# Performance work log

Measured on AMD Instinct MI355X. Metric: run time of the kernel, lower is better.

## Reference

```python
import jax, jax.numpy as jnp
import numpy as np

NUM_EMBEDDINGS = 512
EMBEDDING_DIM = 64
COMMITMENT_COST = 0.25
DECAY = 0.99
EPSILON = 1e-05


def setup_inputs() -> dict:
    key = jax.random.key(0)
    k1, k2, k3 = jax.random.split(key, 3)
    inputs = jax.random.normal(k1, (32, 64, 64, EMBEDDING_DIM), dtype=jnp.float32)
    emb_w = jax.random.normal(k2, (NUM_EMBEDDINGS, EMBEDDING_DIM), dtype=jnp.float32)
    ema_cluster_size = jnp.ones((NUM_EMBEDDINGS,), dtype=jnp.float32)
    ema_w = jax.random.normal(k3, (NUM_EMBEDDINGS, EMBEDDING_DIM), dtype=jnp.float32)
    return {"inputs": inputs, "emb_w": emb_w,
            "ema_cluster_size": ema_cluster_size, "ema_w": ema_w}


def reference(inputs, emb_w, ema_cluster_size, ema_w):
    """VQ-VAE EMA quantizer forward (training=True path).

    inputs:           [B, H, W, D]  NHWC latents
    emb_w:            [K, D]        codebook (pre-update)
    ema_cluster_size: [K]           EMA cluster-size buffer
    ema_w:            [K, D]        EMA weight buffer
    """
    B, H, W, D = inputs.shape
    K = emb_w.shape[0]
    flat = inputs.reshape(-1, D)                                  # [N, D]

    distances = (jnp.sum(flat * flat, axis=1, keepdims=True)
                 - 2.0 * flat @ emb_w.T
                 + jnp.sum(emb_w * emb_w, axis=1))
    encoding_indices = jnp.argmin(distances, axis=1)              # [N]
    encodings = jax.nn.one_hot(encoding_indices, K, dtype=flat.dtype)  # [N, K]

    # --- EMA codebook update (buffer math; no gradient flows here) ---
    counts = jax.lax.stop_gradient(jnp.sum(encodings, axis=0))    # [K]
    cs = ema_cluster_size * DECAY + (1.0 - DECAY) * counts
    n = jnp.sum(cs)
    cs = (cs + EPSILON) / (n + K * EPSILON) * n                   # Laplace smoothing
    dw = jax.ops.segment_sum(jax.lax.stop_gradient(flat),
                             encoding_indices, num_segments=K)    # [K, D]
    new_ema_w = ema_w * DECAY + (1.0 - DECAY) * dw
    new_emb = new_ema_w / cs[:, None]                             # updated codebook

    # Quantize with the updated codebook (gather)
    quantized = new_emb[encoding_indices].reshape(B, H, W, D)

    # Commitment loss (quantized is detached)
    e_latent_loss = jnp.mean((jax.lax.stop_gradient(quantized) - inputs) ** 2)
    loss = COMMITMENT_COST * e_latent_loss

    # Straight-through estimator
    quantized_st = inputs + jax.lax.stop_gradient(quantized - inputs)

    avg_probs = jnp.mean(encodings, axis=0)
    perplexity = jnp.exp(-jnp.sum(avg_probs * jnp.log(avg_probs + 1e-10)))

    # NHWC -> NCHW as in the original return
    return loss, jnp.transpose(quantized_st, (0, 3, 1, 2)), perplexity, encodings
```

## Files before the change

### kernel.cpp

```cpp
#include <hip/hip_runtime.h>

#define DIM 64
#define K_CODES 512
#define N_VEC 131072
#define CREP 16
#define DREP 64
#define Q_OFF 1
#define PERP_OFF 8388609
#define ENC_OFF 8388610

#define DW_BLOCKS 512
#define ENC_BLOCKS 1280

using bfrag = __attribute__((ext_vector_type(8))) short;
using ffrag = __attribute__((ext_vector_type(4))) float;

__device__ __forceinline__ void split3(float x, short& h0, short& h1, short& h2)
{
    unsigned u0 = __float_as_uint(x);
    h0 = (short)(u0 >> 16);
    float r = x - __uint_as_float(u0 & 0xFFFF0000u);
    unsigned u1 = __float_as_uint(r);
    h1 = (short)(u1 >> 16);
    float r2 = r - __uint_as_float(u1 & 0xFFFF0000u);
    h2 = (short)(__float_as_uint(r2) >> 16);
}

__global__ __launch_bounds__(256) void epack_ee_kernel(
    const float* __restrict__ emb_w,
    bfrag* __restrict__ epack,
    float* __restrict__ ee,
    float* __restrict__ crep,
    float* __restrict__ lossac)
{
    __shared__ float part[2][16][8];
    const int tl = threadIdx.x;
    const int t = blockIdx.x * 256 + tl;
    const int lane = t & 63;
    const int db = (t >> 6) & 1;
    const int ctl = tl >> 7;
    const int ct = t >> 7;
    const int r16 = lane & 15, quad = lane >> 4;
    const int c  = ct * 16 + r16;
    const int d0 = db * 32 + quad * 8;
    const float* src = emb_w + (size_t)c * DIM + d0;

    crep[t] = 0.f;
    crep[4096 + t] = 0.f;
    if (t == 0) lossac[0] = 0.f;

    bfrag f0, f1, f2;
    float ssum = 0.f;
#pragma unroll
    for (int j = 0; j < 8; ++j) {
        const float x = src[j];
        ssum = fmaf(x, x, ssum);
        short a, b, cc;
        split3(x, a, b, cc);
        f0[j] = a; f1[j] = b; f2[j] = cc;
    }
    const int base = (ct * 2 + db) * 3;
    epack[(base + 0) * 64 + lane] = f0;
    epack[(base + 1) * 64 + lane] = f1;
    epack[(base + 2) * 64 + lane] = f2;

    part[ctl][r16][db * 4 + quad] = ssum;
    __syncthreads();
    if (tl < 32) {
        const int cl = tl >> 4, r = tl & 15;
        float s = 0.f;
#pragma unroll
        for (int i = 0; i < 8; ++i) s += part[cl][r][i];
        ee[(blockIdx.x * 2 + cl) * 16 + r] = s;
    }
}

__global__ __launch_bounds__(256, 2) void argmin_mfma_kernel(
    const float* __restrict__ inputs,
    const bfrag* __restrict__ epack,
    const float* __restrict__ eeg,
    int* __restrict__ idx,
    float* __restrict__ counts_rep,
    float* __restrict__ dwrep)
{
    const int t = threadIdx.x;
    const int lane = t & 63;
    const int r16 = lane & 15;
    const int quad = lane >> 4;
    const size_t v0 = (size_t)blockIdx.x * 256 + (t >> 6) * 64;

    {
        float4* z4 = reinterpret_cast<float4*>(dwrep) + (size_t)blockIdx.x * 1024;
        const float4 z = make_float4(0.f, 0.f, 0.f, 0.f);
#pragma unroll
        for (int i = 0; i < 4; ++i) z4[i * 256 + t] = z;
    }

    bfrag xf[4][2][3];
#pragma unroll
    for (int rt = 0; rt < 4; ++rt)
#pragma unroll
        for (int db = 0; db < 2; ++db) {
            const float* src = inputs + (v0 + rt * 16 + r16) * DIM + db * 32 + quad * 8;
            const float4 va = *reinterpret_cast<const float4*>(src);
            const float4 vb = *reinterpret_cast<const float4*>(src + 4);
            float vals[8] = {va.x, va.y, va.z, va.w, vb.x, vb.y, vb.z, vb.w};
            bfrag f0, f1, f2;
#pragma unroll
            for (int j = 0; j < 8; ++j) {
                short a, b, c;
                split3(vals[j], a, b, c);
                f0[j] = a; f1[j] = b; f2[j] = c;
            }
            xf[rt][db][0] = f0; xf[rt][db][1] = f1; xf[rt][db][2] = f2;
        }

    float best[4][4];
    int bestk[4][4];
#pragma unroll
    for (int a = 0; a < 4; ++a)
#pragma unroll
        for (int b = 0; b < 4; ++b) { best[a][b] = 3.4e38f; bestk[a][b] = 0; }

    constexpr int PI[6] = {0, 0, 1, 0, 2, 1};
    constexpr int PJ[6] = {0, 1, 0, 2, 0, 1};

#pragma unroll 2
    for (int ct = 0; ct < 32; ++ct) {
        bfrag e[2][3];
#pragma unroll
        for (int db = 0; db < 2; ++db)
#pragma unroll
            for (int s = 0; s < 3; ++s)
                e[db][s] = epack[((ct * 2 + db) * 3 + s) * 64 + lane];
        const float eel = eeg[ct * 16 + r16];

        ffrag acc[4];
#pragma unroll
        for (int rt = 0; rt < 4; ++rt) acc[rt] = (ffrag){0.f, 0.f, 0.f, 0.f};

#pragma unroll
        for (int db = 0; db < 2; ++db)
#pragma unroll
            for (int p = 0; p < 6; ++p)
#pragma unroll
                for (int rt = 0; rt < 4; ++rt)
                    acc[rt] = __builtin_amdgcn_mfma_f32_16x16x32_bf16(
                        xf[rt][db][PI[p]], e[db][PJ[p]], acc[rt], 0, 0, 0);

        const int kc = ct * 16 + r16;
#pragma unroll
        for (int rt = 0; rt < 4; ++rt)
#pragma unroll
            for (int rg = 0; rg < 4; ++rg) {
                const float dist = fmaf(-2.f, acc[rt][rg], eel);
                if (dist < best[rt][rg]) { best[rt][rg] = dist; bestk[rt][rg] = kc; }
            }
    }

#pragma unroll
    for (int rt = 0; rt < 4; ++rt)
#pragma unroll
        for (int rg = 0; rg < 4; ++rg) {
            float b = best[rt][rg];
            int k = bestk[rt][rg];
#pragma unroll
            for (int m = 1; m < 16; m <<= 1) {
                const float ob = __shfl_xor(b, m, 64);
                const int ok = __shfl_xor(k, m, 64);
                if (ob < b || (ob == b && ok < k)) { b = ob; k = ok; }
            }
            bestk[rt][rg] = k;
        }

    if (r16 == 0) {
        float* crep = counts_rep + (blockIdx.x & (CREP - 1)) * K_CODES;
#pragma unroll
        for (int rt = 0; rt < 4; ++rt)
#pragma unroll
            for (int rg = 0; rg < 4; ++rg) {
                const int v = rt * 16 + quad * 4 + rg;
                const int k = bestk[rt][rg];
                idx[v0 + v] = k;
                atomicAdd(&crep[k], 1.0f);
            }
    }
}

__global__ __launch_bounds__(256) void encdw_kernel(
    const float* __restrict__ inputs,
    const int* __restrict__ idx,
    float* __restrict__ enc,
    float* __restrict__ dwrep)
{
    const int bid = blockIdx.x;
    const int t = threadIdx.x;

    if (bid < DW_BLOCKS) {
        __shared__ int sIdx[256];
        const size_t vbase = (size_t)bid * 256;
        sIdx[t] = idx[vbase + t];
        __syncthreads();
        const int w = t >> 6, lane = t & 63;
        const int v0 = w * 64;
#pragma unroll 4
        for (int j = 0; j < 64; ++j) {
            const int v = v0 + j;
            const int k = sIdx[v];
            const float xv = inputs[(vbase + v) * DIM + lane];
            atomicAdd(&dwrep[((size_t)(v & (DREP - 1)) << 15) + (k << 6) + lane], xv);
        }
    } else {
        const int eb = bid - DW_BLOCKS;
        const size_t nf4 = 16777215;
        float4* body = reinterpret_cast<float4*>(enc + 2);
        const size_t stride = (size_t)ENC_BLOCKS * 256;

        for (size_t g = (size_t)eb * 256 + t; g < nf4; g += stride) {
            const size_t e0 = 4 * g + 2;
            const int r0 = (int)(e0 >> 9);
            const int r1 = (int)((e0 + 3) >> 9);
            const int i0 = idx[r0];
            const int i1 = (r1 != r0) ? idx[r1] : i0;
            float4 v;
            v.x = ((int)(e0 & 511) == i0) ? 1.f : 0.f;
            v.y = ((int)((e0 + 1) & 511) == (((e0 + 1) >> 9) == (size_t)r0 ? i0 : i1)) ? 1.f : 0.f;
            v.z = ((int)((e0 + 2) & 511) == (((e0 + 2) >> 9) == (size_t)r0 ? i0 : i1)) ? 1.f : 0.f;
            v.w = ((int)((e0 + 3) & 511) == (((e0 + 3) >> 9) == (size_t)r0 ? i0 : i1)) ? 1.f : 0.f;
            body[g] = v;
        }

        if (eb == 0 && t == 0) {
            const int k0 = idx[0];
            enc[0] = (k0 == 0) ? 1.f : 0.f;
            enc[1] = (k0 == 1) ? 1.f : 0.f;
            const int kL = idx[N_VEC - 1];
            enc[67108862] = (kL == 510) ? 1.f : 0.f;
            enc[67108863] = (kL == 511) ? 1.f : 0.f;
        }
    }
}

__global__ __launch_bounds__(512) void emaA_kernel(
    const float* __restrict__ counts_rep,
    const float* __restrict__ ema_cs,
    float* __restrict__ csbuf,
    float* __restrict__ perp_out)
{
    __shared__ float red[K_CODES];
    const int k = threadIdx.x;
    float cnt = 0.f;
#pragma unroll
    for (int r = 0; r < CREP; ++r) cnt += counts_rep[r * K_CODES + k];
    float cs = ema_cs[k] * 0.99f + 0.01f * cnt;

    red[k] = cs;
    __syncthreads();
    for (int s = K_CODES / 2; s > 0; s >>= 1) {
        if (k < s) red[k] += red[k + s];
        __syncthreads();
    }
    const float n = red[0];
    __syncthreads();

    csbuf[k] = (cs + 1e-5f) / (n + (float)K_CODES * 1e-5f) * n;

    const float p = cnt * (1.0f / (float)N_VEC);
    red[k] = p * logf(p + 1e-10f);
    __syncthreads();
    for (int s = K_CODES / 2; s > 0; s >>= 1) {
        if (k < s) red[k] += red[k + s];
        __syncthreads();
    }
    if (k == 0) perp_out[0] = expf(-red[0]);
}

__global__ __launch_bounds__(256) void emaB_kernel(
    const float* __restrict__ dwrep,
    const float* __restrict__ ema_w,
    const float* __restrict__ csbuf,
    float* __restrict__ new_emb)
{
    const int t = blockIdx.x * 256 + threadIdx.x;
    const int k = t >> 6;
    float dwv = 0.f;
#pragma unroll
    for (int r = 0; r < DREP; ++r) dwv += dwrep[((size_t)r << 15) + t];
    const float v = ema_w[t] * 0.99f + 0.01f * dwv;
    new_emb[t] = v / csbuf[k];
}

__global__ __launch_bounds__(256) void quantize_kernel(
    const float* __restrict__ inputs,
    const int* __restrict__ idx,
    const float* __restrict__ new_emb,
    float* __restrict__ out_q,
    float* __restrict__ loss_accum)
{
    __shared__ int sIdx[64];
    __shared__ float tile[DIM][65];
    __shared__ float wsum[4];

    const int bh = blockIdx.x;
    const int b = bh >> 6, h = bh & 63;
    const int t = threadIdx.x;

    if (t < 64) sIdx[t] = idx[bh * 64 + t];
    __syncthreads();

    const float* inRow = inputs + (size_t)bh * 64 * DIM;
    const int d = t & 63;
    const int wg = t >> 6;
    float lsum = 0.f;
#pragma unroll
    for (int p = 0; p < 16; ++p) {
        const int w = wg * 16 + p;
        const float xv = inRow[w * DIM + d];
        const float qv = new_emb[sIdx[w] * DIM + d];
        const float diff = qv - xv;
        tile[d][w] = xv + diff;
        lsum = fmaf(diff, diff, lsum);
    }
    __syncthreads();

    const int w2 = t & 63;
    const int dg = t >> 6;
#pragma unroll
    for (int p = 0; p < 16; ++p) {
        const int d2 = dg * 16 + p;
        out_q[(((size_t)b * DIM + d2) * 64 + h) * 64 + w2] = tile[d2][w2];
    }

    for (int off = 32; off > 0; off >>= 1) lsum += __shfl_down(lsum, off);
    if ((t & 63) == 0) wsum[t >> 6] = lsum;
    __syncthreads();
    if (t == 0) atomicAdd(loss_accum, (wsum[0] + wsum[1]) + (wsum[2] + wsum[3]));
}

__global__ void finalize_kernel(const float* __restrict__ loss_accum,
                                float* __restrict__ out_loss)
{
    out_loss[0] = 0.25f * (loss_accum[0] / 8388608.0f);
}

extern "C" void kernel_launch(void* const* d_in, const int* in_sizes, int n_in,
                              void* d_out, int out_size, void* d_ws, size_t ws_size,
                              hipStream_t stream)
{
    const float* inputs = (const float*)d_in[0];
    const float* emb_w  = (const float*)d_in[1];
    const float* ema_cs = (const float*)d_in[2];
    const float* ema_w  = (const float*)d_in[3];
    float* out = (float*)d_out;
    float* ws  = (float*)d_ws;

    int*   idxbuf  = (int*)ws;
    float* crep    = ws + 131072;
    float* lossac  = ws + 139264;
    float* csbuf   = ws + 139265;
    float* eebuf   = ws + 139777;
    float* nemb    = ws + 140289;
    bfrag* epack   = (bfrag*)(ws + 173060);

    float* dwrep = out + 16;

    epack_ee_kernel<<<16, 256, 0, stream>>>(emb_w, epack, eebuf, crep, lossac);

    argmin_mfma_kernel<<<N_VEC / 256, 256, 0, stream>>>(
        inputs, epack, eebuf, idxbuf, crep, dwrep);

    encdw_kernel<<<DW_BLOCKS + ENC_BLOCKS, 256, 0, stream>>>(
        inputs, idxbuf, out + ENC_OFF, dwrep);

    emaA_kernel<<<1, K_CODES, 0, stream>>>(crep, ema_cs, csbuf, out + PERP_OFF);
    emaB_kernel<<<K_CODES * DIM / 256, 256, 0, stream>>>(dwrep, ema_w, csbuf, nemb);

    quantize_kernel<<<32 * 64, 256, 0, stream>>>(
        inputs, idxbuf, nemb, out + Q_OFF, lossac);

    finalize_kernel<<<1, 1, 0, stream>>>(lossac, out);
}
```

Before: 184.3 us.

## Split one-hot encoding writes across dw and quantize kernels; fuse EMA kernels

Splits the large one-hot encoding store into two parts. The first is interleaved with the segment-sum atomics and the second is co-scheduled with the quantize/transpose kernel, so bandwidth-bound stores overlap with atomic-bound and gather work. The two EMA kernels are merged into one: each block redundantly recomputes the cluster-size reduction and only block 0 computes perplexity, which saves a launch. The cost is a heavier mix of block types within each kernel and redundant small reductions.

New measurement: 185.8 us. Within noise of the previous version (+0.8%).

```diff
diff --git a/kernel.cpp b/kernel.cpp
--- a/kernel.cpp
+++ b/kernel.cpp
@@ -9,8 +9,12 @@
 #define PERP_OFF 8388609
 #define ENC_OFF 8388610
 
+#define NF4_TOTAL 16777215
+#define ENC_A_F4  9437184
+#define ENC_A_BLOCKS 768
+#define ENC_B_BLOCKS 768
 #define DW_BLOCKS 512
-#define ENC_BLOCKS 1280
+#define QZ_BLOCKS 2048
 
 using bfrag = __attribute__((ext_vector_type(8))) short;
 using ffrag = __attribute__((ext_vector_type(4))) float;
@@ -187,17 +191,39 @@
     }
 }
 
-__global__ __launch_bounds__(256) void encdw_kernel(
+__device__ __forceinline__ void enc_body_write(
+    const int* __restrict__ idx, float* __restrict__ enc,
+    int eb, int nblocks, size_t g_lo, size_t g_hi, int t)
+{
+    float4* body = reinterpret_cast<float4*>(enc + 2);
+    const size_t stride = (size_t)nblocks * 256;
+    for (size_t g = g_lo + (size_t)eb * 256 + t; g < g_hi; g += stride) {
+        const size_t e0 = 4 * g + 2;
+        const int r0 = (int)(e0 >> 9);
+        const int r1 = (int)((e0 + 3) >> 9);
+        const int i0 = idx[r0];
+        const int i1 = (r1 != r0) ? idx[r1] : i0;
+        float4 v;
+        v.x = ((int)(e0 & 511) == i0) ? 1.f : 0.f;
+        v.y = ((int)((e0 + 1) & 511) == (((e0 + 1) >> 9) == (size_t)r0 ? i0 : i1)) ? 1.f : 0.f;
+        v.z = ((int)((e0 + 2) & 511) == (((e0 + 2) >> 9) == (size_t)r0 ? i0 : i1)) ? 1.f : 0.f;
+        v.w = ((int)((e0 + 3) & 511) == (((e0 + 3) >> 9) == (size_t)r0 ? i0 : i1)) ? 1.f : 0.f;
+        body[g] = v;
+    }
+}
+
+__global__ __launch_bounds__(256) void mix1_kernel(
     const float* __restrict__ inputs,
     const int* __restrict__ idx,
     float* __restrict__ enc,
     float* __restrict__ dwrep)
 {
-    const int bid = blockIdx.x;
+    const int g = blockIdx.x / 5, r = blockIdx.x % 5;
     const int t = threadIdx.x;
 
-    if (bid < DW_BLOCKS) {
+    if (r < 2) {
         __shared__ int sIdx[256];
+        const int bid = g * 2 + r;
         const size_t vbase = (size_t)bid * 256;
         sIdx[t] = idx[vbase + t];
         __syncthreads();
@@ -211,130 +237,130 @@
             atomicAdd(&dwrep[((size_t)(v & (DREP - 1)) << 15) + (k << 6) + lane], xv);
         }
     } else {
-        const int eb = bid - DW_BLOCKS;
-        const size_t nf4 = 16777215;
-        float4* body = reinterpret_cast<float4*>(enc + 2);
-        const size_t stride = (size_t)ENC_BLOCKS * 256;
-
-        for (size_t g = (size_t)eb * 256 + t; g < nf4; g += stride) {
-            const size_t e0 = 4 * g + 2;
-            const int r0 = (int)(e0 >> 9);
-            const int r1 = (int)((e0 + 3) >> 9);
-            const int i0 = idx[r0];
-            const int i1 = (r1 != r0) ? idx[r1] : i0;
-            float4 v;
-            v.x = ((int)(e0 & 511) == i0) ? 1.f : 0.f;
-            v.y = ((int)((e0 + 1) & 511) == (((e0 + 1) >> 9) == (size_t)r0 ? i0 : i1)) ? 1.f : 0.f;
-            v.z = ((int)((e0 + 2) & 511) == (((e0 + 2) >> 9) == (size_t)r0 ? i0 : i1)) ? 1.f : 0.f;
-            v.w = ((int)((e0 + 3) & 511) == (((e0 + 3) >> 9) == (size_t)r0 ? i0 : i1)) ? 1.f : 0.f;
-            body[g] = v;
-        }
-
+        const int eb = g * 3 + (r - 2);
+        enc_body_write(idx, enc, eb, ENC_A_BLOCKS, 0, ENC_A_F4, t);
         if (eb == 0 && t == 0) {
             const int k0 = idx[0];
             enc[0] = (k0 == 0) ? 1.f : 0.f;
             enc[1] = (k0 == 1) ? 1.f : 0.f;
-            const int kL = idx[N_VEC - 1];
-            enc[67108862] = (kL == 510) ? 1.f : 0.f;
-            enc[67108863] = (kL == 511) ? 1.f : 0.f;
-        }
-    }
-}
-
-__global__ __launch_bounds__(512) void emaA_kernel(
+        }
+    }
+}
+
+__global__ __launch_bounds__(256) void emaBF_kernel(
     const float* __restrict__ counts_rep,
     const float* __restrict__ ema_cs,
-    float* __restrict__ csbuf,
+    const float* __restrict__ dwrep,
+    const float* __restrict__ ema_w,
+    float* __restrict__ new_emb,
     float* __restrict__ perp_out)
 {
-    __shared__ float red[K_CODES];
-    const int k = threadIdx.x;
-    float cnt = 0.f;
-#pragma unroll
-    for (int r = 0; r < CREP; ++r) cnt += counts_rep[r * K_CODES + k];
-    float cs = ema_cs[k] * 0.99f + 0.01f * cnt;
-
-    red[k] = cs;
+    __shared__ float scs[K_CODES];
+    __shared__ float red[256];
+    const int t = threadIdx.x;
+
+    float c0 = 0.f, c1 = 0.f;
+#pragma unroll
+    for (int r = 0; r < CREP; ++r) {
+        c0 += counts_rep[r * K_CODES + 2 * t];
+        c1 += counts_rep[r * K_CODES + 2 * t + 1];
+    }
+    const float cs0 = ema_cs[2 * t] * 0.99f + 0.01f * c0;
+    const float cs1 = ema_cs[2 * t + 1] * 0.99f + 0.01f * c1;
+
+    red[t] = cs0 + cs1;
     __syncthreads();
-    for (int s = K_CODES / 2; s > 0; s >>= 1) {
-        if (k < s) red[k] += red[k + s];
+    for (int s = 128; s > 0; s >>= 1) {
+        if (t < s) red[t] += red[t + s];
         __syncthreads();
     }
     const float n = red[0];
     __syncthreads();
 
-    csbuf[k] = (cs + 1e-5f) / (n + (float)K_CODES * 1e-5f) * n;
-
-    const float p = cnt * (1.0f / (float)N_VEC);
-    red[k] = p * logf(p + 1e-10f);
+    const float scale = n / (n + (float)K_CODES * 1e-5f);
+    scs[2 * t]     = (cs0 + 1e-5f) * scale;
+    scs[2 * t + 1] = (cs1 + 1e-5f) * scale;
+
+    if (blockIdx.x == 0) {
+        const float p0 = c0 * (1.0f / (float)N_VEC);
+        const float p1 = c1 * (1.0f / (float)N_VEC);
+        red[t] = p0 * logf(p0 + 1e-10f) + p1 * logf(p1 + 1e-10f);
+        __syncthreads();
+        for (int s = 128; s > 0; s >>= 1) {
+            if (t < s) red[t] += red[t + s];
+            __syncthreads();
+        }
+        if (t == 0) perp_out[0] = expf(-red[0]);
+    }
     __syncthreads();
-    for (int s = K_CODES / 2; s > 0; s >>= 1) {
-        if (k < s) red[k] += red[k + s];
-        __syncthreads();
-    }
-    if (k == 0) perp_out[0] = expf(-red[0]);
-}
-
-__global__ __launch_bounds__(256) void emaB_kernel(
-    const float* __restrict__ dwrep,
-    const float* __restrict__ ema_w,
-    const float* __restrict__ csbuf,
-    float* __restrict__ new_emb)
-{
-    const int t = blockIdx.x * 256 + threadIdx.x;
-    const int k = t >> 6;
+
+    const int k = blockIdx.x * 4 + (t >> 6);
+    const int e = k * DIM + (t & 63);
     float dwv = 0.f;
 #pragma unroll
-    for (int r = 0; r < DREP; ++r) dwv += dwrep[((size_t)r << 15) + t];
-    const float v = ema_w[t] * 0.99f + 0.01f * dwv;
-    new_emb[t] = v / csbuf[k];
-}
-
-__global__ __launch_bounds__(256) void quantize_kernel(
+    for (int r = 0; r < DREP; ++r) dwv += dwrep[((size_t)r << 15) + e];
+    const float v = ema_w[e] * 0.99f + 0.01f * dwv;
+    new_emb[e] = v / scs[k];
+}
+
+__global__ __launch_bounds__(256) void mix2_kernel(
     const float* __restrict__ inputs,
     const int* __restrict__ idx,
     const float* __restrict__ new_emb,
     float* __restrict__ out_q,
-    float* __restrict__ loss_accum)
-{
-    __shared__ int sIdx[64];
-    __shared__ float tile[DIM][65];
-    __shared__ float wsum[4];
-
-    const int bh = blockIdx.x;
-    const int b = bh >> 6, h = bh & 63;
+    float* __restrict__ loss_accum,
+    float* __restrict__ enc)
+{
+    const int g = blockIdx.x / 11, r = blockIdx.x % 11;
     const int t = threadIdx.x;
 
-    if (t < 64) sIdx[t] = idx[bh * 64 + t];
-    __syncthreads();
-
-    const float* inRow = inputs + (size_t)bh * 64 * DIM;
-    const int d = t & 63;
-    const int wg = t >> 6;
-    float lsum = 0.f;
-#pragma unroll
-    for (int p = 0; p < 16; ++p) {
-        const int w = wg * 16 + p;
-        const float xv = inRow[w * DIM + d];
-        const float qv = new_emb[sIdx[w] * DIM + d];
-        const float diff = qv - xv;
-        tile[d][w] = xv + diff;
-        lsum = fmaf(diff, diff, lsum);
-    }
-    __syncthreads();
-
-    const int w2 = t & 63;
-    const int dg = t >> 6;
-#pragma unroll
-    for (int p = 0; p < 16; ++p) {
-        const int d2 = dg * 16 + p;
-        out_q[(((size_t)b * DIM + d2) * 64 + h) * 64 + w2] = tile[d2][w2];
-    }
-
-    for (int off = 32; off > 0; off >>= 1) lsum += __shfl_down(lsum, off);
-    if ((t & 63) == 0) wsum[t >> 6] = lsum;
-    __syncthreads();
-    if (t == 0) atomicAdd(loss_accum, (wsum[0] + wsum[1]) + (wsum[2] + wsum[3]));
+    if (r < 8) {
+        __shared__ int sIdx[64];
+        __shared__ float tile[DIM][65];
+        __shared__ float wsum[4];
+
+        const int bh = g * 8 + r;
+        const int b = bh >> 6, h = bh & 63;
+
+        if (t < 64) sIdx[t] = idx[bh * 64 + t];
+        __syncthreads();
+
+        const float* inRow = inputs + (size_t)bh * 64 * DIM;
+        const int d = t & 63;
+        const int wg = t >> 6;
+        float lsum = 0.f;
+#pragma unroll
+        for (int p = 0; p < 16; ++p) {
+            const int w = wg * 16 + p;
+            const float xv = inRow[w * DIM + d];
+            const float qv = new_emb[sIdx[w] * DIM + d];
+            const float diff = qv - xv;
+            tile[d][w] = xv + diff;
+            lsum = fmaf(diff, diff, lsum);
+        }
+        __syncthreads();
+
+        const int w2 = t & 63;
+        const int dg = t >> 6;
+#pragma unroll
+        for (int p = 0; p < 16; ++p) {
+            const int d2 = dg * 16 + p;
+            out_q[(((size_t)b * DIM + d2) * 64 + h) * 64 + w2] = tile[d2][w2];
+        }
+
+        for (int off = 32; off > 0; off >>= 1) lsum += __shfl_down(lsum, off);
+        if ((t & 63) == 0) wsum[t >> 6] = lsum;
+        __syncthreads();
+        if (t == 0) atomicAdd(loss_accum, (wsum[0] + wsum[1]) + (wsum[2] + wsum[3]));
+    } else {
+        const int eb = g * 3 + (r - 8);
+        enc_body_write(idx, enc, eb, ENC_B_BLOCKS, ENC_A_F4, NF4_TOTAL, t);
+        if (eb == 0 && t == 0) {
+            const int kL = idx[N_VEC - 1];
+            enc[67108862] = (kL == 510) ? 1.f : 0.f;
+            enc[67108863] = (kL == 511) ? 1.f : 0.f;
+        }
+    }
 }
 
 __global__ void finalize_kernel(const float* __restrict__ loss_accum,
@@ -361,6 +387,7 @@
     float* eebuf   = ws + 139777;
     float* nemb    = ws + 140289;
     bfrag* epack   = (bfrag*)(ws + 173060);
+    (void)csbuf;
 
     float* dwrep = out + 16;
 
@@ -369,14 +396,14 @@
     argmin_mfma_kernel<<<N_VEC / 256, 256, 0, stream>>>(
         inputs, epack, eebuf, idxbuf, crep, dwrep);
 
-    encdw_kernel<<<DW_BLOCKS + ENC_BLOCKS, 256, 0, stream>>>(
+    mix1_kernel<<<DW_BLOCKS + ENC_A_BLOCKS, 256, 0, stream>>>(
         inputs, idxbuf, out + ENC_OFF, dwrep);
 
-    emaA_kernel<<<1, K_CODES, 0, stream>>>(crep, ema_cs, csbuf, out + PERP_OFF);
-    emaB_kernel<<<K_CODES * DIM / 256, 256, 0, stream>>>(dwrep, ema_w, csbuf, nemb);
-
-    quantize_kernel<<<32 * 64, 256, 0, stream>>>(
-        inputs, idxbuf, nemb, out + Q_OFF, lossac);
+    emaBF_kernel<<<K_CODES / 4, 256, 0, stream>>>(
+        crep, ema_cs, dwrep, ema_w, nemb, out + PERP_OFF);
+
+    mix2_kernel<<<QZ_BLOCKS + ENC_B_BLOCKS, 256, 0, stream>>>(
+        inputs, idxbuf, nemb, out + Q_OFF, lossac, out + ENC_OFF);
 
     finalize_kernel<<<1, 1, 0, stream>>>(lossac, out);
 }
```
